# Kernel optimization log

Hardware: AMD Instinct MI355X
Metric: run time of the kernel (lower is better)

## Reference

```python
import jax, jax.numpy as jnp
from jax import lax
import numpy as np

B, T, H = 256, 256, 256  # batch, seq_len, hidden per direction
IN0 = 4                  # one-hot DNA bases


def setup_inputs() -> dict:
    key = jax.random.key(0)
    ks = jax.random.split(key, 12)
    s = 1.0 / np.sqrt(H)  # PyTorch GRU init scale
    return {
        "x": jax.random.normal(ks[0], (B, T, IN0), jnp.float32),
        "Wih0": jax.random.normal(ks[1], (2, 3 * H, IN0), jnp.float32) * s,
        "Whh0": jax.random.normal(ks[2], (2, 3 * H, H), jnp.float32) * s,
        "bih0": jax.random.normal(ks[3], (2, 3 * H), jnp.float32) * s,
        "bhh0": jax.random.normal(ks[4], (2, 3 * H), jnp.float32) * s,
        "Wih1": jax.random.normal(ks[5], (2, 3 * H, 2 * H), jnp.float32) * s,
        "Whh1": jax.random.normal(ks[6], (2, 3 * H, H), jnp.float32) * s,
        "bih1": jax.random.normal(ks[7], (2, 3 * H), jnp.float32) * s,
        "bhh1": jax.random.normal(ks[8], (2, 3 * H), jnp.float32) * s,
        "W_out": jax.random.normal(ks[9], (3, H), jnp.float32) * s,
        "b_out": jax.random.normal(ks[10], (3,), jnp.float32) * s,
    }


def _gru_dir(x, Wih, Whh, bih, bhh, reverse):
    """One direction of a GRU layer. x: [B,T,F] -> [B,T,H]."""
    # Precompute input projections for all timesteps: [T, B, 3H]
    xp = jnp.swapaxes(jnp.einsum('btf,gf->btg', x, Wih) + bih, 0, 1)
    h0 = jnp.zeros((x.shape[0], H), x.dtype)

    def step(h, xpt):
        gh = h @ Whh.T + bhh
        xr, xz, xn = jnp.split(xpt, 3, axis=-1)
        hr, hz, hn = jnp.split(gh, 3, axis=-1)
        r = jax.nn.sigmoid(xr + hr)
        z = jax.nn.sigmoid(xz + hz)
        n = jnp.tanh(xn + r * hn)
        h_new = (1.0 - z) * n + z * h
        return h_new, h_new

    _, hs = lax.scan(step, h0, xp, reverse=reverse)  # hs: [T,B,H] in time order
    return jnp.swapaxes(hs, 0, 1)


def _bigru_layer(x, Wih, Whh, bih, bhh):
    fwd = _gru_dir(x, Wih[0], Whh[0], bih[0], bhh[0], reverse=False)
    bwd = _gru_dir(x, Wih[1], Whh[1], bih[1], bhh[1], reverse=True)
    return jnp.concatenate([fwd, bwd], axis=-1)  # [B,T,2H]


def reference(x, Wih0, Whh0, bih0, bhh0, Wih1, Whh1, bih1, bhh1, W_out, b_out):
    h1 = _bigru_layer(x, Wih0, Whh0, bih0, bhh0)   # [B,T,2H]
    h2 = _bigru_layer(h1, Wih1, Whh1, bih1, bhh1)  # [B,T,2H]
    # sum forward/backward halves, then take last timestep
    out = h2[:, :, :H] + h2[:, :, H:]              # [B,T,H]
    last = out[:, -1, :]                           # [B,H]
    logits = last @ W_out.T + b_out                # [B,3]
    return jax.nn.softmax(logits, axis=1)
```

## Files before the change

kernel.cpp:

```cpp
#include <hip/hip_runtime.h>


typedef __attribute__((ext_vector_type(8))) short short8;
typedef __attribute__((ext_vector_type(4))) short sh4;
typedef __attribute__((ext_vector_type(4))) float f32x4;

__device__ __forceinline__ short f2bf(float f) {
  union { float f; unsigned u; } v; v.f = f;
  unsigned r = v.u + 0x7fffu + ((v.u >> 16) & 1u);
  return (short)(r >> 16);
}
__device__ __forceinline__ float bf2f(unsigned short b) {
  union { unsigned u; float f; } v; v.u = ((unsigned)b) << 16; return v.f;
}
__device__ __forceinline__ float sigf(float x) {
  return __builtin_amdgcn_rcpf(1.f + __expf(-x));
}
__device__ __forceinline__ float tanhf_(float x) {
  return 1.f - 2.f * __builtin_amdgcn_rcpf(1.f + __expf(2.f * x));
}
__device__ __forceinline__ void gload_lds16(const void* g, void* s) {
  __builtin_amdgcn_global_load_lds(
      (const __attribute__((address_space(1))) unsigned int*)g,
      (__attribute__((address_space(3))) unsigned int*)s, 16, 0, 0);
}
#define US4_GET(v, i) ((i) == 0 ? (v).x : (i) == 1 ? (v).y : (i) == 2 ? (v).z : (v).w)

__global__ __launch_bounds__(256) void prep_wf(
    const float* __restrict__ whh0, const float* __restrict__ whh1,
    const float* __restrict__ wih0, const float* __restrict__ bih0,
    const float* __restrict__ bhh0, const float* __restrict__ bhh1,
    short* __restrict__ whhf, short* __restrict__ wextf) {
  int tid = blockIdx.x * 256 + threadIdx.x;
  if (tid < 73728) {
    int l = tid & 63;
    int rest = tid >> 6;
    int kk = rest & 7;
    int rest2 = rest >> 3;
    int nt = rest2 % 48;
    int m  = rest2 / 48;
    int row = nt * 16 + (l & 15);
    int k0  = kk * 32 + (l >> 4) * 8;
    const float* src = (m < 2) ? (whh0 + (size_t)m * 768 * 256) : whh1;
    const float* p = src + (size_t)row * 256 + k0;
    short8 o;
    #pragma unroll
    for (int s = 0; s < 8; ++s) o[s] = f2bf(p[s]);
    ((short8*)whhf)[tid] = o;
  } else {
    int j = tid - 73728;
    int l = j & 63;
    int tt = (j >> 6) & 15;
    int grp = (j >> 10) & 3;
    int m = j >> 12;
    int l15 = l & 15, lhi = l >> 4;
    int gate = (grp <= 1) ? grp : 2;
    int row = gate * 256 + tt * 16 + l15;
    short8 o = {};
    #pragma unroll
    for (int s = 0; s < 8; ++s) {
      int c = lhi * 8 + s;
      float v = 0.f;
      if (grp == 2) {
        if (c == 4) v = (m < 2) ? bhh0[m * 768 + row] : bhh1[row];
      } else if (m < 2) {
        if (c < 4) v = wih0[((size_t)m * 768 + row) * 4 + c];
        else if (c == 4) {
          v = bih0[m * 768 + row];
          if (grp < 2) v += bhh0[m * 768 + row];
        }
      }
      o[s] = f2bf(v);
    }
    ((short8*)wextf)[j] = o;
  }
}

__global__ __launch_bounds__(256) void prep_w1b(const float* __restrict__ wih1,
                                                short* __restrict__ out) {
  int i = blockIdx.x * 256 + threadIdx.x;
  const float* p = wih1 + (size_t)i * 8;
  short8 o;
  #pragma unroll
  for (int s = 0; s < 8; ++s) o[s] = f2bf(p[s]);
  ((short8*)out)[i] = o;
}

template <int LAYER>
__global__ __launch_bounds__(512, 2) void gru_step(
    const float* __restrict__ x,
    const short* __restrict__ wf,
    const unsigned short* __restrict__ xp1g,
    short* __restrict__ h0c,
    float* __restrict__ hfl) {
  const int wg  = blockIdx.x;
  const int dir = (LAYER == 0) ? (wg >> 4) : 0;
  const int bt  = (LAYER == 0) ? (wg & 15) : wg;
  const int b0  = bt * 16;
  const int tid = threadIdx.x;
  const int w = tid >> 6, l = tid & 63, l15 = l & 15, lhi = l >> 4;
  const int mat = (LAYER == 0) ? dir : 2;
  const short* wext = wf + 589824;

  __shared__ __align__(16) short wlds[49152];
  __shared__ __align__(16) short hb[2][4096];
  __shared__ __align__(16) short ext2[2][640];

  #pragma unroll
  for (int t6 = 0; t6 < 6; ++t6) {
    const int g = t6 >> 1, s = t6 & 1;
    const int tile = g * 16 + 2 * w + s;
    #pragma unroll
    for (int kkl = 0; kkl < 2; ++kkl)
      gload_lds16(wf + (((size_t)(mat * 48 + tile) * 8) + 6 + kkl) * 512 + l * 8,
                  &wlds[((w * 6 + t6) * 2 + kkl) * 512]);
  }

  for (int i = tid; i < 4096; i += 512) hb[0][i] = 0;
  for (int i = tid; i < 1280; i += 512) ((short*)ext2)[i] = 0;

  short8 wreg[3][2][6];
  #pragma unroll
  for (int g = 0; g < 3; ++g)
    #pragma unroll
    for (int s = 0; s < 2; ++s) {
      const int tile = g * 16 + 2 * w + s;
      #pragma unroll
      for (int kk = 0; kk < 6; ++kk)
        wreg[g][s][kk] = ((const short8*)wf)[((size_t)(mat * 48 + tile) * 8 + kk) * 64 + l];
    }
  short8 aext[4][2];
  #pragma unroll
  for (int grp = 0; grp < 4; ++grp) {
    if (LAYER == 1 && grp != 2) continue;
    #pragma unroll
    for (int s = 0; s < 2; ++s)
      aext[grp][s] = ((const short8*)wext)[((size_t)(mat * 4 + grp) * 16 + 2 * w + s) * 64 + l];
  }

  __syncthreads();
  if (LAYER == 0 && tid < 16) {
    const int t0 = dir ? 255 : 0;
    float4 xe = ((const float4*)x)[(size_t)(b0 + tid) * 256 + t0];
    short8 e = {};
    e[0] = f2bf(xe.x); e[1] = f2bf(xe.y); e[2] = f2bf(xe.z); e[3] = f2bf(xe.w);
    e[4] = (short)0x3F80;
    *(short8*)&ext2[0][tid * 40] = e;
  }
  float hreg[2][4] = {{0, 0, 0, 0}, {0, 0, 0, 0}};
  __syncthreads();

  for (int t = 0; t < 256; ++t) {
    const int cur = t & 1;

    if (LAYER == 0 && tid < 16 && t < 255) {
      const int tn = dir ? 254 - t : t + 1;
      float4 xe = ((const float4*)x)[(size_t)(b0 + tid) * 256 + tn];
      short8 e = {};
      e[0] = f2bf(xe.x); e[1] = f2bf(xe.y); e[2] = f2bf(xe.z); e[3] = f2bf(xe.w);
      e[4] = (short)0x3F80;
      *(short8*)&ext2[cur ^ 1][tid * 40] = e;
    }

    ushort4 xq[3][2];
    if (LAYER == 1) {
      const unsigned short* base = xp1g + ((size_t)t * 256 + (b0 + l15)) * 768;
      #pragma unroll
      for (int g = 0; g < 3; ++g)
        #pragma unroll
        for (int s = 0; s < 2; ++s)
          xq[g][s] = *(const ushort4*)(base + g * 256 + 32 * w + 16 * s + lhi * 4);
    }

    if (LAYER == 0 && t > 0) {
      const int tprev = dir ? 256 - t : t - 1;
      const int br = tid >> 5, c = tid & 31;
      short8 v = *(const short8*)&hb[cur][br * 256 + ((c ^ (br & 7)) << 3)];
      __builtin_nontemporal_store(v,
          (short8*)(h0c + ((size_t)(b0 + br) * 256 + tprev) * 512 + dir * 256 + c * 8));
    }

    f32x4 acc[3][2] = {};
    f32x4 accx[2] = {};
    #pragma unroll
    for (int kk = 0; kk < 8; ++kk) {
      const int gidx = kk * 4 + lhi;
      const short8 bfr = *(const short8*)&hb[cur][l15 * 256 + ((gidx ^ (l15 & 7)) << 3)];
      if (kk < 6) {
        #pragma unroll
        for (int g = 0; g < 3; ++g)
          #pragma unroll
          for (int s = 0; s < 2; ++s)
            acc[g][s] = __builtin_amdgcn_mfma_f32_16x16x32_bf16(wreg[g][s][kk], bfr, acc[g][s], 0, 0, 0);
      } else {
        #pragma unroll
        for (int g = 0; g < 3; ++g)
          #pragma unroll
          for (int s = 0; s < 2; ++s) {
            const short8 wl =
                *(const short8*)&wlds[((w * 6 + g * 2 + s) * 2 + (kk - 6)) * 512 + l * 8];
            acc[g][s] = __builtin_amdgcn_mfma_f32_16x16x32_bf16(wl, bfr, acc[g][s], 0, 0, 0);
          }
      }
    }
    short8 bext;
    if (LAYER == 0) {
      bext = *(const short8*)&ext2[cur][l15 * 40 + lhi * 8];
    } else {
      short8 e = {};
      if (lhi == 0) e[4] = (short)0x3F80;
      bext = e;
    }
    if (LAYER == 0) {
      #pragma unroll
      for (int s = 0; s < 2; ++s) {
        acc[0][s] = __builtin_amdgcn_mfma_f32_16x16x32_bf16(aext[0][s], bext, acc[0][s], 0, 0, 0);
        acc[1][s] = __builtin_amdgcn_mfma_f32_16x16x32_bf16(aext[1][s], bext, acc[1][s], 0, 0, 0);
        acc[2][s] = __builtin_amdgcn_mfma_f32_16x16x32_bf16(aext[2][s], bext, acc[2][s], 0, 0, 0);
        accx[s]   = __builtin_amdgcn_mfma_f32_16x16x32_bf16(aext[3][s], bext, accx[s], 0, 0, 0);
      }
    } else {
      #pragma unroll
      for (int s = 0; s < 2; ++s)
        acc[2][s] = __builtin_amdgcn_mfma_f32_16x16x32_bf16(aext[2][s], bext, acc[2][s], 0, 0, 0);
    }

    #pragma unroll
    for (int s = 0; s < 2; ++s) {
      float hv[4];
      #pragma unroll
      for (int i = 0; i < 4; ++i) {
        float r, z, n;
        if (LAYER == 0) {
          r = sigf(acc[0][s][i]);
          z = sigf(acc[1][s][i]);
          n = tanhf_(accx[s][i] + r * acc[2][s][i]);
        } else {
          r = sigf(acc[0][s][i] + bf2f(US4_GET(xq[0][s], i)));
          z = sigf(acc[1][s][i] + bf2f(US4_GET(xq[1][s], i)));
          n = tanhf_(bf2f(US4_GET(xq[2][s], i)) + r * acc[2][s][i]);
        }
        const float h = n + z * (hreg[s][i] - n);
        hreg[s][i] = h;
        hv[i] = h;
      }
      const int gsw = 4 * w + 2 * s + (lhi >> 1);
      const int so = l15 * 256 + ((gsw ^ (l15 & 7)) << 3) + (lhi & 1) * 4;
      unsigned p01 = (unsigned)(unsigned short)f2bf(hv[0]) |
                     ((unsigned)(unsigned short)f2bf(hv[1]) << 16);
      unsigned p23 = (unsigned)(unsigned short)f2bf(hv[2]) |
                     ((unsigned)(unsigned short)f2bf(hv[3]) << 16);
      uint2 pk; pk.x = p01; pk.y = p23;
      *(uint2*)&hb[cur ^ 1][so] = pk;
    }
    __syncthreads();
  }

  if (LAYER == 0) {
    const int tlast = dir ? 0 : 255;
    const int br = tid >> 5, c = tid & 31;
    short8 v = *(const short8*)&hb[0][br * 256 + ((c ^ (br & 7)) << 3)];
    __builtin_nontemporal_store(v,
        (short8*)(h0c + ((size_t)(b0 + br) * 256 + tlast) * 512 + dir * 256 + c * 8));
  } else {
    #pragma unroll
    for (int s = 0; s < 2; ++s)
      #pragma unroll
      for (int i = 0; i < 4; ++i)
        hfl[(size_t)(b0 + l15) * 256 + 32 * w + 16 * s + lhi * 4 + i] = hreg[s][i];
  }
}

__global__ __launch_bounds__(256, 2) void xp1_gemm(
    const short* __restrict__ h0c, const short* __restrict__ w1b,
    const float* __restrict__ bih1, const float* __restrict__ bhh1,
    unsigned short* __restrict__ xp1g) {
  const int mb = blockIdx.x, nb = blockIdx.y;
  const int tid = threadIdx.x;
  const int w = tid >> 6, l = tid & 63, l15 = l & 15, lhi = l >> 4;
  const int wm = w >> 1, wn = w & 1;
  __shared__ __align__(16) short As[128 * 64];
  __shared__ __align__(16) short Bs[128 * 64];
  f32x4 acc[4][4] = {};

  for (int ks = 0; ks < 8; ++ks) {
    short8 sa[4], sb[4];
    #pragma unroll
    for (int c = 0; c < 4; ++c) {
      int li = w * 256 + c * 64 + l;
      int row = li >> 3, cgr = li & 7;
      sa[c] = *(const short8*)(h0c + (size_t)(mb * 128 + row) * 512 + ks * 64 + cgr * 8);
      sb[c] = *(const short8*)(w1b + (size_t)(nb * 128 + row) * 512 + ks * 64 + cgr * 8);
    }
    __syncthreads();
    #pragma unroll
    for (int c = 0; c < 4; ++c) {
      int li = w * 256 + c * 64 + l;
      int row = li >> 3, cgr = li & 7;
      int sl = ((cgr ^ (row & 7)) << 3);
      *(short8*)&As[row * 64 + sl] = sa[c];
      *(short8*)&Bs[row * 64 + sl] = sb[c];
    }
    __syncthreads();
    short8 af[4][2], bfr[4][2];
    #pragma unroll
    for (int mt = 0; mt < 4; ++mt)
      #pragma unroll
      for (int kk = 0; kk < 2; ++kk) {
        int row = wm * 64 + mt * 16 + l15;
        int g = kk * 4 + lhi;
        af[mt][kk] = *(const short8*)&As[row * 64 + ((g ^ (row & 7)) << 3)];
      }
    #pragma unroll
    for (int nt2 = 0; nt2 < 4; ++nt2)
      #pragma unroll
      for (int kk = 0; kk < 2; ++kk) {
        int row = wn * 64 + nt2 * 16 + l15;
        int g = kk * 4 + lhi;
        bfr[nt2][kk] = *(const short8*)&Bs[row * 64 + ((g ^ (row & 7)) << 3)];
      }
    #pragma unroll
    for (int kk = 0; kk < 2; ++kk)
      #pragma unroll
      for (int mt = 0; mt < 4; ++mt)
        #pragma unroll
        for (int nt2 = 0; nt2 < 4; ++nt2)
          acc[mt][nt2] = __builtin_amdgcn_mfma_f32_16x16x32_bf16(
              af[mt][kk], bfr[nt2][kk], acc[mt][nt2], 0, 0, 0);
  }

  #pragma unroll
  for (int nt2 = 0; nt2 < 4; ++nt2) {
    const int gate = nb * 128 + wn * 64 + nt2 * 16 + l15;
    const float bias = bih1[gate] + ((gate < 512) ? bhh1[gate] : 0.f);
    #pragma unroll
    for (int mt = 0; mt < 4; ++mt)
      #pragma unroll
      for (int i = 0; i < 4; ++i) {
        const int rt = mb * 128 + wm * 64 + mt * 16 + lhi * 4 + i;
        const int b = rt >> 8, tt = rt & 255;
        xp1g[((size_t)tt * 256 + b) * 768 + gate] =
            (unsigned short)f2bf(acc[mt][nt2][i] + bias);
      }
  }
}

__global__ __launch_bounds__(256) void bwd255(
    const short* __restrict__ h0c, const float* __restrict__ wih1,
    const float* __restrict__ bih1, const float* __restrict__ bhh1,
    float* __restrict__ hb) {
  const int b = blockIdx.x, j = threadIdx.x;
  __shared__ __align__(16) float hrow[512];
  const unsigned short* hr = (const unsigned short*)(h0c + (size_t)(b * 256 + 255) * 512);
  for (int k = j; k < 512; k += 256) hrow[k] = bf2f(hr[k]);
  __syncthreads();
  const float4* hr4 = (const float4*)hrow;
  float g[3];
  #pragma unroll
  for (int gi = 0; gi < 3; ++gi) {
    const float4* wr = (const float4*)(wih1 + (size_t)768 * 512 + (size_t)(gi * 256 + j) * 512);
    float s = 0.f;
    #pragma unroll 4
    for (int k = 0; k < 128; ++k) {
      float4 aq = hr4[k], bq = wr[k];
      s += aq.x * bq.x + aq.y * bq.y + aq.z * bq.z + aq.w * bq.w;
    }
    g[gi] = s + bih1[768 + gi * 256 + j];
  }
  float r = sigf(g[0] + bhh1[768 + j]);
  float z = sigf(g[1] + bhh1[768 + 256 + j]);
  float n = tanhf_(g[2] + r * bhh1[768 + 512 + j]);
  hb[b * 256 + j] = (1.f - z) * n;
}

__global__ __launch_bounds__(64) void head(
    const float* __restrict__ hf, const float* __restrict__ hb,
    const float* __restrict__ wout, const float* __restrict__ bout,
    float* __restrict__ out) {
  const int b = blockIdx.x, l = threadIdx.x;
  float s0 = 0.f, s1 = 0.f, s2 = 0.f;
  for (int k = l; k < 256; k += 64) {
    float v = hf[b * 256 + k] + hb[b * 256 + k];
    s0 += v * wout[k];
    s1 += v * wout[256 + k];
    s2 += v * wout[512 + k];
  }
  #pragma unroll
  for (int off = 32; off > 0; off >>= 1) {
    s0 += __shfl_down(s0, off);
    s1 += __shfl_down(s1, off);
    s2 += __shfl_down(s2, off);
  }
  if (l == 0) {
    s0 += bout[0]; s1 += bout[1]; s2 += bout[2];
    float m = fmaxf(s0, fmaxf(s1, s2));
    float e0 = __expf(s0 - m), e1 = __expf(s1 - m), e2 = __expf(s2 - m);
    float inv = 1.f / (e0 + e1 + e2);
    out[b * 3 + 0] = e0 * inv;
    out[b * 3 + 1] = e1 * inv;
    out[b * 3 + 2] = e2 * inv;
  }
}

extern "C" void kernel_launch(void* const* d_in, const int* in_sizes, int n_in,
                              void* d_out, int out_size, void* d_ws, size_t ws_size,
                              hipStream_t stream) {
  const float* x    = (const float*)d_in[0];
  const float* wih0 = (const float*)d_in[1];
  const float* whh0 = (const float*)d_in[2];
  const float* bih0 = (const float*)d_in[3];
  const float* bhh0 = (const float*)d_in[4];
  const float* wih1 = (const float*)d_in[5];
  const float* whh1 = (const float*)d_in[6];
  const float* bih1 = (const float*)d_in[7];
  const float* bhh1 = (const float*)d_in[8];
  const float* wout = (const float*)d_in[9];
  const float* bout = (const float*)d_in[10];
  float* out = (float*)d_out;

  char* ws = (char*)d_ws;
  short* whhf           = (short*)(ws + 0);
  short* wextf          = (short*)(ws + 1179648);
  short* w1b            = (short*)(ws + 1376256);
  short* h0c            = (short*)(ws + 2162688);
  unsigned short* xp1g  = (unsigned short*)(ws + 69271552);
  float* hb255          = (float*)(ws + 169934848);
  float* hfl            = (float*)(ws + 170196992);

  prep_wf<<<336, 256, 0, stream>>>(whh0, whh1, wih0, bih0, bhh0, bhh1, whhf, wextf);
  prep_w1b<<<192, 256, 0, stream>>>(wih1, w1b);
  gru_step<0><<<32, 512, 0, stream>>>(x, whhf, nullptr, h0c, nullptr);
  bwd255<<<256, 256, 0, stream>>>(h0c, wih1, bih1, bhh1, hb255);
  xp1_gemm<<<dim3(512, 6), 256, 0, stream>>>(h0c, w1b, bih1, bhh1, xp1g);
  gru_step<1><<<16, 512, 0, stream>>>(nullptr, whhf, xp1g, nullptr, hfl);
  head<<<256, 64, 0, stream>>>(hfl, hb255, wout, bout, out);
}
```

Baseline: 1.330 ms.

## Split GRU recurrence across twice as many workgroups with 8 batch rows each

The recurrent GRU kernels now use 256-thread workgroups covering 8 batch rows instead of 512-thread groups covering 16. This doubles the grid to 64 and 32 workgroups, so more CUs share the serial time loop. Each wave now holds twice as many weight tiles in registers, pinned there with empty asm barriers. The MFMA B operand is still 16 wide, so half its columns are padding and MFMA work per useful row doubles. That also raises register pressure, with a risk of spills at occupancy 1.

```diff
diff --git a/kernel.cpp b/kernel.cpp
--- a/kernel.cpp
+++ b/kernel.cpp
@@ -2,7 +2,6 @@
 
 
 typedef __attribute__((ext_vector_type(8))) short short8;
-typedef __attribute__((ext_vector_type(4))) short sh4;
 typedef __attribute__((ext_vector_type(4))) float f32x4;
 
 __device__ __forceinline__ short f2bf(float f) {
@@ -87,16 +86,17 @@
 }
 
 template <int LAYER>
-__global__ __launch_bounds__(512, 2) void gru_step(
+__global__ __launch_bounds__(256, 1) void gru_step(
     const float* __restrict__ x,
     const short* __restrict__ wf,
     const unsigned short* __restrict__ xp1g,
     short* __restrict__ h0c,
     float* __restrict__ hfl) {
+  constexpr int ROWS = 8;
   const int wg  = blockIdx.x;
-  const int dir = (LAYER == 0) ? (wg >> 4) : 0;
-  const int bt  = (LAYER == 0) ? (wg & 15) : wg;
-  const int b0  = bt * 16;
+  const int dir = (LAYER == 0) ? (wg >> 5) : 0;
+  const int bt  = (LAYER == 0) ? (wg & 31) : wg;
+  const int b0  = bt * ROWS;
   const int tid = threadIdx.x;
   const int w = tid >> 6, l = tid & 63, l15 = l & 15, lhi = l >> 4;
   const int mat = (LAYER == 0) ? dir : 2;
@@ -107,39 +107,49 @@
   __shared__ __align__(16) short ext2[2][640];
 
   #pragma unroll
-  for (int t6 = 0; t6 < 6; ++t6) {
-    const int g = t6 >> 1, s = t6 & 1;
-    const int tile = g * 16 + 2 * w + s;
-    #pragma unroll
-    for (int kkl = 0; kkl < 2; ++kkl)
-      gload_lds16(wf + (((size_t)(mat * 48 + tile) * 8) + 6 + kkl) * 512 + l * 8,
-                  &wlds[((w * 6 + t6) * 2 + kkl) * 512]);
-  }
-
-  for (int i = tid; i < 4096; i += 512) hb[0][i] = 0;
-  for (int i = tid; i < 1280; i += 512) ((short*)ext2)[i] = 0;
-
-  short8 wreg[3][2][6];
+  for (int r = 0; r < 24; ++r) {
+    const int Bb = r * 4 + w;
+    gload_lds16(wf + ((size_t)(mat * 48 + (Bb >> 1)) * 8 + 6 + (Bb & 1)) * 512 + l * 8,
+                &wlds[Bb * 512]);
+  }
+  for (int i = tid; i < 8192; i += 256) ((short*)hb)[i] = 0;
+  for (int i = tid; i < 1280; i += 256) ((short*)ext2)[i] = 0;
+
+  short8 wreg[3][4][6];
   #pragma unroll
   for (int g = 0; g < 3; ++g)
     #pragma unroll
-    for (int s = 0; s < 2; ++s) {
-      const int tile = g * 16 + 2 * w + s;
+    for (int j = 0; j < 4; ++j) {
+      const int tile = g * 16 + 4 * w + j;
       #pragma unroll
       for (int kk = 0; kk < 6; ++kk)
-        wreg[g][s][kk] = ((const short8*)wf)[((size_t)(mat * 48 + tile) * 8 + kk) * 64 + l];
-    }
-  short8 aext[4][2];
-  #pragma unroll
-  for (int grp = 0; grp < 4; ++grp) {
-    if (LAYER == 1 && grp != 2) continue;
-    #pragma unroll
-    for (int s = 0; s < 2; ++s)
-      aext[grp][s] = ((const short8*)wext)[((size_t)(mat * 4 + grp) * 16 + 2 * w + s) * 64 + l];
-  }
+        wreg[g][j][kk] = ((const short8*)wf)[((size_t)(mat * 48 + tile) * 8 + kk) * 64 + l];
+    }
+  short8 aext[4][4];
+  #pragma unroll
+  for (int grp = 0; grp < 4; ++grp)
+    #pragma unroll
+    for (int j = 0; j < 4; ++j) {
+      if (LAYER == 1 && grp != 2) continue;
+      aext[grp][j] = ((const short8*)wext)[((size_t)(mat * 4 + grp) * 16 + 4 * w + j) * 64 + l];
+    }
+  #pragma unroll
+  for (int g = 0; g < 3; ++g)
+    #pragma unroll
+    for (int j = 0; j < 4; ++j)
+      #pragma unroll
+      for (int kk = 0; kk < 6; ++kk)
+        asm volatile("" : "+v"(wreg[g][j][kk]));
+  #pragma unroll
+  for (int grp = 0; grp < 4; ++grp)
+    #pragma unroll
+    for (int j = 0; j < 4; ++j) {
+      if (LAYER == 1 && grp != 2) continue;
+      asm volatile("" : "+v"(aext[grp][j]));
+    }
 
   __syncthreads();
-  if (LAYER == 0 && tid < 16) {
+  if (LAYER == 0 && tid < ROWS) {
     const int t0 = dir ? 255 : 0;
     float4 xe = ((const float4*)x)[(size_t)(b0 + tid) * 256 + t0];
     short8 e = {};
@@ -147,13 +157,13 @@
     e[4] = (short)0x3F80;
     *(short8*)&ext2[0][tid * 40] = e;
   }
-  float hreg[2][4] = {{0, 0, 0, 0}, {0, 0, 0, 0}};
+  float hreg[4][4] = {};
   __syncthreads();
 
   for (int t = 0; t < 256; ++t) {
     const int cur = t & 1;
 
-    if (LAYER == 0 && tid < 16 && t < 255) {
+    if (LAYER == 0 && tid < ROWS && t < 255) {
       const int tn = dir ? 254 - t : t + 1;
       float4 xe = ((const float4*)x)[(size_t)(b0 + tid) * 256 + tn];
       short8 e = {};
@@ -162,14 +172,14 @@
       *(short8*)&ext2[cur ^ 1][tid * 40] = e;
     }
 
-    ushort4 xq[3][2];
+    ushort4 xq[3][4];
     if (LAYER == 1) {
-      const unsigned short* base = xp1g + ((size_t)t * 256 + (b0 + l15)) * 768;
+      const unsigned short* base = xp1g + ((size_t)t * 256 + (b0 + (l15 & 7))) * 768;
       #pragma unroll
       for (int g = 0; g < 3; ++g)
         #pragma unroll
-        for (int s = 0; s < 2; ++s)
-          xq[g][s] = *(const ushort4*)(base + g * 256 + 32 * w + 16 * s + lhi * 4);
+        for (int j = 0; j < 4; ++j)
+          xq[g][j] = *(const ushort4*)(base + g * 256 + 64 * w + 16 * j + lhi * 4);
     }
 
     if (LAYER == 0 && t > 0) {
@@ -180,8 +190,8 @@
           (short8*)(h0c + ((size_t)(b0 + br) * 256 + tprev) * 512 + dir * 256 + c * 8));
     }
 
-    f32x4 acc[3][2] = {};
-    f32x4 accx[2] = {};
+    f32x4 acc[3][4] = {};
+    f32x4 accx[4] = {};
     #pragma unroll
     for (int kk = 0; kk < 8; ++kk) {
       const int gidx = kk * 4 + lhi;
@@ -190,68 +200,65 @@
         #pragma unroll
         for (int g = 0; g < 3; ++g)
           #pragma unroll
-          for (int s = 0; s < 2; ++s)
-            acc[g][s] = __builtin_amdgcn_mfma_f32_16x16x32_bf16(wreg[g][s][kk], bfr, acc[g][s], 0, 0, 0);
+          for (int j = 0; j < 4; ++j)
+            acc[g][j] = __builtin_amdgcn_mfma_f32_16x16x32_bf16(wreg[g][j][kk], bfr, acc[g][j], 0, 0, 0);
       } else {
         #pragma unroll
         for (int g = 0; g < 3; ++g)
           #pragma unroll
-          for (int s = 0; s < 2; ++s) {
-            const short8 wl =
-                *(const short8*)&wlds[((w * 6 + g * 2 + s) * 2 + (kk - 6)) * 512 + l * 8];
-            acc[g][s] = __builtin_amdgcn_mfma_f32_16x16x32_bf16(wl, bfr, acc[g][s], 0, 0, 0);
+          for (int j = 0; j < 4; ++j) {
+            const int tile = g * 16 + 4 * w + j;
+            const short8 wl = *(const short8*)&wlds[(tile * 2 + (kk - 6)) * 512 + l * 8];
+            acc[g][j] = __builtin_amdgcn_mfma_f32_16x16x32_bf16(wl, bfr, acc[g][j], 0, 0, 0);
           }
       }
     }
-    short8 bext;
     if (LAYER == 0) {
-      bext = *(const short8*)&ext2[cur][l15 * 40 + lhi * 8];
+      const short8 bext = *(const short8*)&ext2[cur][l15 * 40 + lhi * 8];
+      #pragma unroll
+      for (int j = 0; j < 4; ++j) {
+        acc[0][j] = __builtin_amdgcn_mfma_f32_16x16x32_bf16(aext[0][j], bext, acc[0][j], 0, 0, 0);
+        acc[1][j] = __builtin_amdgcn_mfma_f32_16x16x32_bf16(aext[1][j], bext, acc[1][j], 0, 0, 0);
+        acc[2][j] = __builtin_amdgcn_mfma_f32_16x16x32_bf16(aext[2][j], bext, acc[2][j], 0, 0, 0);
+        accx[j]   = __builtin_amdgcn_mfma_f32_16x16x32_bf16(aext[3][j], bext, accx[j], 0, 0, 0);
+      }
     } else {
       short8 e = {};
       if (lhi == 0) e[4] = (short)0x3F80;
-      bext = e;
-    }
-    if (LAYER == 0) {
-      #pragma unroll
-      for (int s = 0; s < 2; ++s) {
-        acc[0][s] = __builtin_amdgcn_mfma_f32_16x16x32_bf16(aext[0][s], bext, acc[0][s], 0, 0, 0);
-        acc[1][s] = __builtin_amdgcn_mfma_f32_16x16x32_bf16(aext[1][s], bext, acc[1][s], 0, 0, 0);
-        acc[2][s] = __builtin_amdgcn_mfma_f32_16x16x32_bf16(aext[2][s], bext, acc[2][s], 0, 0, 0);
-        accx[s]   = __builtin_amdgcn_mfma_f32_16x16x32_bf16(aext[3][s], bext, accx[s], 0, 0, 0);
-      }
-    } else {
-      #pragma unroll
-      for (int s = 0; s < 2; ++s)
-        acc[2][s] = __builtin_amdgcn_mfma_f32_16x16x32_bf16(aext[2][s], bext, acc[2][s], 0, 0, 0);
-    }
-
-    #pragma unroll
-    for (int s = 0; s < 2; ++s) {
+      #pragma unroll
+      for (int j = 0; j < 4; ++j)
+        acc[2][j] = __builtin_amdgcn_mfma_f32_16x16x32_bf16(aext[2][j], e, acc[2][j], 0, 0, 0);
+    }
+
+    #pragma unroll
+    for (int j = 0; j < 4; ++j) {
       float hv[4];
       #pragma unroll
       for (int i = 0; i < 4; ++i) {
         float r, z, n;
         if (LAYER == 0) {
-          r = sigf(acc[0][s][i]);
-          z = sigf(acc[1][s][i]);
-          n = tanhf_(accx[s][i] + r * acc[2][s][i]);
+          r = sigf(acc[0][j][i]);
+          z = sigf(acc[1][j][i]);
+          n = tanhf_(accx[j][i] + r * acc[2][j][i]);
         } else {
-          r = sigf(acc[0][s][i] + bf2f(US4_GET(xq[0][s], i)));
-          z = sigf(acc[1][s][i] + bf2f(US4_GET(xq[1][s], i)));
-          n = tanhf_(bf2f(US4_GET(xq[2][s], i)) + r * acc[2][s][i]);
+          r = sigf(acc[0][j][i] + bf2f(US4_GET(xq[0][j], i)));
+          z = sigf(acc[1][j][i] + bf2f(US4_GET(xq[1][j], i)));
+          n = tanhf_(bf2f(US4_GET(xq[2][j], i)) + r * acc[2][j][i]);
         }
-        const float h = n + z * (hreg[s][i] - n);
-        hreg[s][i] = h;
+        const float h = n + z * (hreg[j][i] - n);
+        hreg[j][i] = h;
         hv[i] = h;
       }
-      const int gsw = 4 * w + 2 * s + (lhi >> 1);
-      const int so = l15 * 256 + ((gsw ^ (l15 & 7)) << 3) + (lhi & 1) * 4;
-      unsigned p01 = (unsigned)(unsigned short)f2bf(hv[0]) |
-                     ((unsigned)(unsigned short)f2bf(hv[1]) << 16);
-      unsigned p23 = (unsigned)(unsigned short)f2bf(hv[2]) |
-                     ((unsigned)(unsigned short)f2bf(hv[3]) << 16);
-      uint2 pk; pk.x = p01; pk.y = p23;
-      *(uint2*)&hb[cur ^ 1][so] = pk;
+      if (l15 < ROWS) {
+        const int gsw = 8 * w + 2 * j + (lhi >> 1);
+        const int so = l15 * 256 + ((gsw ^ (l15 & 7)) << 3) + (lhi & 1) * 4;
+        unsigned p01 = (unsigned)(unsigned short)f2bf(hv[0]) |
+                       ((unsigned)(unsigned short)f2bf(hv[1]) << 16);
+        unsigned p23 = (unsigned)(unsigned short)f2bf(hv[2]) |
+                       ((unsigned)(unsigned short)f2bf(hv[3]) << 16);
+        uint2 pk; pk.x = p01; pk.y = p23;
+        *(uint2*)&hb[cur ^ 1][so] = pk;
+      }
     }
     __syncthreads();
   }
@@ -262,12 +269,12 @@
     short8 v = *(const short8*)&hb[0][br * 256 + ((c ^ (br & 7)) << 3)];
     __builtin_nontemporal_store(v,
         (short8*)(h0c + ((size_t)(b0 + br) * 256 + tlast) * 512 + dir * 256 + c * 8));
-  } else {
-    #pragma unroll
-    for (int s = 0; s < 2; ++s)
+  } else if (l15 < ROWS) {
+    #pragma unroll
+    for (int j = 0; j < 4; ++j)
       #pragma unroll
       for (int i = 0; i < 4; ++i)
-        hfl[(size_t)(b0 + l15) * 256 + 32 * w + 16 * s + lhi * 4 + i] = hreg[s][i];
+        hfl[(size_t)(b0 + l15) * 256 + 64 * w + 16 * j + lhi * 4 + i] = hreg[j][i];
   }
 }
 
@@ -429,9 +436,9 @@
 
   prep_wf<<<336, 256, 0, stream>>>(whh0, whh1, wih0, bih0, bhh0, bhh1, whhf, wextf);
   prep_w1b<<<192, 256, 0, stream>>>(wih1, w1b);
-  gru_step<0><<<32, 512, 0, stream>>>(x, whhf, nullptr, h0c, nullptr);
+  gru_step<0><<<64, 256, 0, stream>>>(x, whhf, nullptr, h0c, nullptr);
   bwd255<<<256, 256, 0, stream>>>(h0c, wih1, bih1, bhh1, hb255);
   xp1_gemm<<<dim3(512, 6), 256, 0, stream>>>(h0c, w1b, bih1, bhh1, xp1g);
-  gru_step<1><<<16, 512, 0, stream>>>(nullptr, whhf, xp1g, nullptr, hfl);
+  gru_step<1><<<32, 256, 0, stream>>>(nullptr, whhf, xp1g, nullptr, hfl);
   head<<<256, 64, 0, stream>>>(hfl, hb255, wout, bout, out);
 }
```

Result: slower. 1.996 ms (+50.1%).
